# Kernel optimization log

Hardware: AMD Instinct MI355X
Metric: run time of the kernel (lower is better)

The kernel has to match this reference:

```python
import jax, jax.numpy as jnp
import numpy as np

B, T, D = 4, 2048, 512
H, DK = 8, 64  # n_head, d_kv; inner_dim = H*DK = 512


def setup_inputs() -> dict:
    key = jax.random.key(0)
    ks = jax.random.split(key, 6)
    s = 1.0 / np.sqrt(D)
    return {
        "x": jax.random.normal(ks[0], (B, T, D), dtype=jnp.float32),
        "mask": jnp.zeros((B, 1, 1, T), dtype=jnp.float32),
        "position_bias": jax.random.normal(ks[1], (1, H, T, T), dtype=jnp.float32),
        "Wq": jax.random.normal(ks[2], (D, D), dtype=jnp.float32) * s,
        "Wk": jax.random.normal(ks[3], (D, D), dtype=jnp.float32) * s,
        "Wv": jax.random.normal(ks[4], (D, D), dtype=jnp.float32) * s,
        "Wo": jax.random.normal(ks[5], (D, D), dtype=jnp.float32) * s,
    }


def reference(x, mask, position_bias, Wq, Wk, Wv, Wo):
    # Linear projections (torch nn.Linear: y = x @ W.T), split into heads.
    q = (x @ Wq.T).reshape(B, T, H, DK).transpose(0, 2, 1, 3)  # [B,H,T,DK]
    k = (x @ Wk.T).reshape(B, T, H, DK).transpose(0, 2, 1, 3)  # [B,H,S,DK]
    v = (x @ Wv.T).reshape(B, T, H, DK).transpose(0, 2, 1, 3)  # [B,H,S,DK]
    # T5: no 1/sqrt(d_k) scaling; additive position bias + mask before softmax.
    scores = jnp.einsum("bhtd,bhsd->bhts", q, k) + position_bias + mask
    attn = jax.nn.softmax(scores.astype(jnp.float32), axis=-1).astype(q.dtype)
    # dropout is identity at inference
    y = jnp.einsum("bhts,bhsd->bhtd", attn, v)  # [B,H,T,DK]
    y = y.transpose(0, 2, 1, 3).reshape(B, T, H * DK)
    return y @ Wo.T
```

## Files before the change

### kernel.cpp

```cpp
#include <hip/hip_runtime.h>
#include <stdint.h>

typedef unsigned short u16;
typedef __attribute__((ext_vector_type(8))) _Float16 half8;
typedef __attribute__((ext_vector_type(4))) float f32x4;

#define L2E 1.4426950408889634f

#define NTOK 8192
#define DIM  512
#define TT   2048

__device__ __forceinline__ u16 f2h(float f) {
  _Float16 h = (_Float16)f;
  return __builtin_bit_cast(u16, h);
}

__device__ __forceinline__ void async16(const void* g, void* l) {
  __builtin_amdgcn_global_load_lds(
      (const __attribute__((address_space(1))) unsigned int*)g,
      (__attribute__((address_space(3))) unsigned int*)l, 16, 0, 0);
}

__global__ __launch_bounds__(256) void k_convert(
    const float* __restrict__ x, const float* __restrict__ wq,
    const float* __restrict__ wk, const float* __restrict__ wv,
    const float* __restrict__ wo, u16* __restrict__ xb) {
  size_t i = ((size_t)blockIdx.x * 256 + threadIdx.x) * 8;
  const float* src;
  u16* dst;
  size_t off;
  if (i < 4194304) {
    src = x; dst = xb; off = i;
  } else {
    size_t j = i - 4194304;
    int w = (int)(j >> 18);
    off = j & 262143;
    src = (w == 0) ? wq : (w == 1) ? wk : (w == 2) ? wv : wo;
    dst = xb + 4194304 + (size_t)w * 262144;
  }
  float4 a = *(const float4*)(src + off);
  float4 b = *(const float4*)(src + off + 4);
  uint4 pk;
  pk.x = (unsigned)f2h(a.x) | ((unsigned)f2h(a.y) << 16);
  pk.y = (unsigned)f2h(a.z) | ((unsigned)f2h(a.w) << 16);
  pk.z = (unsigned)f2h(b.x) | ((unsigned)f2h(b.y) << 16);
  pk.w = (unsigned)f2h(b.z) | ((unsigned)f2h(b.w) << 16);
  *(uint4*)(dst + off) = pk;
}

template <bool VSWAP>
__global__ __launch_bounds__(256) void k_proj(
    const u16* __restrict__ A, const u16* __restrict__ Wb,
    u16* __restrict__ Db) {
  const int tid = threadIdx.x;
  const int wave = tid >> 6, lane = tid & 63;
  const int quad = lane >> 4, l16 = lane & 15;
  const int wr = wave >> 1, wc = wave & 1;
  const int m0 = blockIdx.x * 128, n0 = blockIdx.y * 128;

  const u16* W;
  u16* D;
  if (VSWAP) {
    W = Wb + 2 * 262144;
    D = Db + 2 * (size_t)4194304;
  } else {
    int z = blockIdx.z;
    W = Wb + (size_t)z * 262144;
    D = Db + (size_t)z * 4194304;
  }

  __shared__ __align__(16) u16 As[128 * 64];
  __shared__ __align__(16) u16 Bs[128 * 64];

  f32x4 acc[4][4];
  for (int rt = 0; rt < 4; ++rt)
    for (int ct = 0; ct < 4; ++ct) acc[rt][ct] = (f32x4){0.f, 0.f, 0.f, 0.f};

  for (int kb = 0; kb < 8; ++kb) {
    const int k0 = kb * 64;
    for (int r = 0; r < 4; ++r) {
      int cid = r * 256 + tid;
      int row = cid >> 3, cl = cid & 7, cg = cl ^ (row & 7);
      async16(A + (size_t)(m0 + row) * DIM + k0 + cg * 8,
              &As[(r * 256 + wave * 64) * 8]);
    }
    for (int r = 0; r < 4; ++r) {
      int cid = r * 256 + tid;
      int row = cid >> 3, cl = cid & 7, cg = cl ^ (row & 7);
      async16(W + (size_t)(n0 + row) * DIM + k0 + cg * 8,
              &Bs[(r * 256 + wave * 64) * 8]);
    }
    __syncthreads();
    for (int kc = 0; kc < 2; ++kc) {
      half8 af[4], wf[4];
      for (int rt = 0; rt < 4; ++rt) {
        int row = wr * 64 + rt * 16 + l16;
        int c = (kc * 4 + quad) ^ (row & 7);
        af[rt] = *(const half8*)&As[row * 64 + c * 8];
      }
      for (int ct = 0; ct < 4; ++ct) {
        int row = wc * 64 + ct * 16 + l16;
        int c = (kc * 4 + quad) ^ (row & 7);
        wf[ct] = *(const half8*)&Bs[row * 64 + c * 8];
      }
      for (int rt = 0; rt < 4; ++rt)
        for (int ct = 0; ct < 4; ++ct)
          acc[rt][ct] = VSWAP
              ? __builtin_amdgcn_mfma_f32_16x16x32_f16(wf[ct], af[rt],
                                                       acc[rt][ct], 0, 0, 0)
              : __builtin_amdgcn_mfma_f32_16x16x32_f16(af[rt], wf[ct],
                                                       acc[rt][ct], 0, 0, 0);
    }
    __syncthreads();
  }

  for (int rt = 0; rt < 4; ++rt)
    for (int ct = 0; ct < 4; ++ct)
      for (int reg = 0; reg < 4; ++reg) {
        float v = acc[rt][ct][reg];
        if (!VSWAP) {
          int gm = m0 + wr * 64 + rt * 16 + quad * 4 + reg;
          int gn = n0 + wc * 64 + ct * 16 + l16;
          int bb = gm >> 11, t = gm & 2047, hh = gn >> 6, dk = gn & 63;
          D[(((size_t)(bb * 8 + hh) * TT + t) << 6) + dk] = f2h(v);
        } else {
          int feat = n0 + wc * 64 + ct * 16 + quad * 4 + reg;
          int tok  = m0 + wr * 64 + rt * 16 + l16;
          int bb = tok >> 11, t = tok & 2047, hh = feat >> 6, dk = feat & 63;
          D[(((size_t)(bb * 8 + hh) << 6) + dk) * TT + t] = f2h(v);
        }
      }
}

__global__ __launch_bounds__(256) void k_ogemm(
    const u16* __restrict__ A, const u16* __restrict__ W,
    float* __restrict__ Df) {
  const int tid = threadIdx.x;
  const int wave = tid >> 6, lane = tid & 63;
  const int quad = lane >> 4, l16 = lane & 15;
  const int wr = wave >> 1, wc = wave & 1;
  const int m0 = blockIdx.x * 64, n0 = blockIdx.y * 128;

  __shared__ __align__(16) u16 As[64 * 64];
  __shared__ __align__(16) u16 Bs[128 * 64];

  f32x4 acc[2][4];
  for (int rt = 0; rt < 2; ++rt)
    for (int ct = 0; ct < 4; ++ct) acc[rt][ct] = (f32x4){0.f, 0.f, 0.f, 0.f};

  for (int kb = 0; kb < 8; ++kb) {
    const int k0 = kb * 64;
    for (int r = 0; r < 2; ++r) {
      int cid = r * 256 + tid;
      int row = cid >> 3, cl = cid & 7, cg = cl ^ (row & 7);
      async16(A + (size_t)(m0 + row) * DIM + k0 + cg * 8,
              &As[(r * 256 + wave * 64) * 8]);
    }
    for (int r = 0; r < 4; ++r) {
      int cid = r * 256 + tid;
      int row = cid >> 3, cl = cid & 7, cg = cl ^ (row & 7);
      async16(W + (size_t)(n0 + row) * DIM + k0 + cg * 8,
              &Bs[(r * 256 + wave * 64) * 8]);
    }
    __syncthreads();
    for (int kc = 0; kc < 2; ++kc) {
      half8 af[2], wf[4];
      for (int rt = 0; rt < 2; ++rt) {
        int row = wr * 32 + rt * 16 + l16;
        int c = (kc * 4 + quad) ^ (row & 7);
        af[rt] = *(const half8*)&As[row * 64 + c * 8];
      }
      for (int ct = 0; ct < 4; ++ct) {
        int row = wc * 64 + ct * 16 + l16;
        int c = (kc * 4 + quad) ^ (row & 7);
        wf[ct] = *(const half8*)&Bs[row * 64 + c * 8];
      }
      for (int rt = 0; rt < 2; ++rt)
        for (int ct = 0; ct < 4; ++ct)
          acc[rt][ct] = __builtin_amdgcn_mfma_f32_16x16x32_f16(
              af[rt], wf[ct], acc[rt][ct], 0, 0, 0);
    }
    __syncthreads();
  }

  for (int rt = 0; rt < 2; ++rt)
    for (int ct = 0; ct < 4; ++ct)
      for (int reg = 0; reg < 4; ++reg) {
        int gm = m0 + wr * 32 + rt * 16 + quad * 4 + reg;
        int gn = n0 + wc * 64 + ct * 16 + l16;
        Df[(size_t)gm * DIM + gn] = acc[rt][ct][reg];
      }
}

__global__ __launch_bounds__(256) void k_attn(
    const u16* __restrict__ Q, const u16* __restrict__ K,
    const u16* __restrict__ Vt, const float* __restrict__ bias,
    const float* __restrict__ mask, u16* __restrict__ Y) {
  const int tid = threadIdx.x;
  const int wv = tid >> 6;
  const int lane = tid & 63;
  const int quad = lane >> 4;
  const int l16 = lane & 15;

  const int bx = blockIdx.x;
  const int bh = bx >> 5;
  const int qt = bx & 31;
  const int b = bh >> 3, h = bh & 7;
  const int q0 = qt * 64;

  __shared__ __align__(16) u16 Ks[64 * 64];
  __shared__ __align__(16) u16 Vs[64 * 64];
  __shared__ __align__(16) u16 Pl[64 * 72];

  half8 qf[2];
  {
    size_t qrow = (size_t)bh * TT + q0 + wv * 16 + l16;
    for (int kc = 0; kc < 2; ++kc)
      qf[kc] = *(const half8*)(Q + qrow * 64 + kc * 32 + quad * 8);
  }

  float m_i[4], l_i[4];
  f32x4 oacc[4];
  for (int r = 0; r < 4; ++r) { m_i[r] = -1e30f; l_i[r] = 0.f; }
  for (int ct = 0; ct < 4; ++ct) oacc[ct] = (f32x4){0.f, 0.f, 0.f, 0.f};

  const size_t biasbase = (size_t)h * TT * TT;

  for (int st = 0; st < 32; ++st) {
    const int s0 = st * 64;
    for (int r = 0; r < 2; ++r) {
      int cid = r * 256 + tid;
      int row = cid >> 3, cl = cid & 7, cg = cl ^ (row & 7);
      async16(K + ((size_t)bh * TT + s0 + row) * 64 + cg * 8,
              &Ks[(r * 256 + wv * 64) * 8]);
      async16(Vt + ((size_t)(bh * 64 + row)) * TT + s0 + cg * 8,
              &Vs[(r * 256 + wv * 64) * 8]);
    }
    __syncthreads();

    float mk[4];
    for (int ct = 0; ct < 4; ++ct) mk[ct] = mask[b * TT + s0 + ct * 16 + l16];

    f32x4 sacc[4];
    for (int ct = 0; ct < 4; ++ct) sacc[ct] = (f32x4){0.f, 0.f, 0.f, 0.f};
    for (int kc = 0; kc < 2; ++kc) {
      half8 kf[4];
      for (int ct = 0; ct < 4; ++ct) {
        int row = ct * 16 + l16;
        int c = (kc * 4 + quad) ^ (row & 7);
        kf[ct] = *(const half8*)&Ks[row * 64 + c * 8];
      }
      for (int ct = 0; ct < 4; ++ct)
        sacc[ct] = __builtin_amdgcn_mfma_f32_16x16x32_f16(
            qf[kc], kf[ct], sacc[ct], 0, 0, 0);
    }

    float bv[4][4];
    {
      int tg = q0 + wv * 16 + quad * 4;
      for (int reg = 0; reg < 4; ++reg) {
        const float* bp = bias + biasbase + (size_t)(tg + reg) * TT + s0 + l16;
        for (int ct = 0; ct < 4; ++ct) bv[ct][reg] = bp[ct * 16];
      }
    }

    for (int reg = 0; reg < 4; ++reg) {
      float s[4];
      for (int ct = 0; ct < 4; ++ct)
        s[ct] = sacc[ct][reg] + bv[ct][reg] + mk[ct];
      float mx = fmaxf(fmaxf(s[0], s[1]), fmaxf(s[2], s[3]));
      mx = fmaxf(mx, __shfl_xor(mx, 1));
      mx = fmaxf(mx, __shfl_xor(mx, 2));
      mx = fmaxf(mx, __shfl_xor(mx, 4));
      mx = fmaxf(mx, __shfl_xor(mx, 8));
      float mold = m_i[reg];
      float mnew = fmaxf(mold, mx);
      float alpha = __builtin_amdgcn_exp2f((mold - mnew) * L2E);
      float p[4], rs = 0.f;
      for (int ct = 0; ct < 4; ++ct) {
        p[ct] = __builtin_amdgcn_exp2f((s[ct] - mnew) * L2E);
        rs += p[ct];
      }
      rs += __shfl_xor(rs, 1);
      rs += __shfl_xor(rs, 2);
      rs += __shfl_xor(rs, 4);
      rs += __shfl_xor(rs, 8);
      l_i[reg] = l_i[reg] * alpha + rs;
      m_i[reg] = mnew;
      for (int ct = 0; ct < 4; ++ct) oacc[ct][reg] *= alpha;
      int prow = wv * 16 + quad * 4 + reg;
      for (int ct = 0; ct < 4; ++ct) Pl[prow * 72 + ct * 16 + l16] = f2h(p[ct]);
    }
    __syncthreads();

    for (int kc = 0; kc < 2; ++kc) {
      half8 pf, vf[4];
      pf = *(const half8*)&Pl[(wv * 16 + l16) * 72 + kc * 32 + quad * 8];
      for (int ct = 0; ct < 4; ++ct) {
        int row = ct * 16 + l16;
        int c = (kc * 4 + quad) ^ (row & 7);
        vf[ct] = *(const half8*)&Vs[row * 64 + c * 8];
      }
      for (int ct = 0; ct < 4; ++ct)
        oacc[ct] = __builtin_amdgcn_mfma_f32_16x16x32_f16(
            pf, vf[ct], oacc[ct], 0, 0, 0);
    }
    __syncthreads();
  }

  for (int reg = 0; reg < 4; ++reg) {
    int tg = q0 + wv * 16 + quad * 4 + reg;
    float inv = 1.f / l_i[reg];
    for (int ct = 0; ct < 4; ++ct) {
      float v = oacc[ct][reg] * inv;
      Y[((size_t)(b * TT + tg)) * DIM + h * 64 + ct * 16 + l16] = f2h(v);
    }
  }
}

extern "C" void kernel_launch(void* const* d_in, const int* in_sizes, int n_in,
                              void* d_out, int out_size, void* d_ws, size_t ws_size,
                              hipStream_t stream) {
  const float* x    = (const float*)d_in[0];
  const float* mask = (const float*)d_in[1];
  const float* bias = (const float*)d_in[2];
  const float* Wq   = (const float*)d_in[3];
  const float* Wk   = (const float*)d_in[4];
  const float* Wv   = (const float*)d_in[5];
  const float* Wo   = (const float*)d_in[6];
  (void)Wk; (void)Wv;

  u16* xb  = (u16*)d_ws;
  u16* wb  = xb + 4194304;
  u16* qkv = wb + 4 * 262144;
  u16* yb  = qkv + 3 * (size_t)4194304;

  k_convert<<<2560, 256, 0, stream>>>(x, Wq, Wk, Wv, Wo, xb);
  k_proj<false><<<dim3(64, 4, 2), 256, 0, stream>>>(xb, wb, qkv);
  k_proj<true><<<dim3(64, 4), 256, 0, stream>>>(xb, wb, qkv);
  k_attn<<<1024, 256, 0, stream>>>(qkv, qkv + 4194304,
                                   qkv + 2 * (size_t)4194304, bias, mask, yb);
  k_ogemm<<<dim3(128, 4), 256, 0, stream>>>(yb, wb + 3 * 262144, (float*)d_out);
}
```

Before: 329.7 us.

## Transpose attention MFMA operands so each lane owns a query row

Swaps the MFMA operand order in the attention kernel so each lane holds one query row across four key columns. Softmax statistics become per-lane scalars reduced with only two cross-lane shuffles, and bias and mask are read as float4 vectors. The next tile's bias is prefetched into registers during the current tile's softmax. The change also replaces a block-wide barrier with a per-wave LDS wait, adds setprio around the MFMA sections and an occupancy hint in launch bounds, and packs P and output stores into 64-bit writes. It risks higher register pressure from the prefetched bias and relies on each wave reading only its own rows of P.

```diff
diff --git a/kernel.cpp b/kernel.cpp
--- a/kernel.cpp
+++ b/kernel.cpp
@@ -193,7 +193,7 @@
       }
 }
 
-__global__ __launch_bounds__(256) void k_attn(
+__global__ __launch_bounds__(256, 4) void k_attn(
     const u16* __restrict__ Q, const u16* __restrict__ K,
     const u16* __restrict__ Vt, const float* __restrict__ bias,
     const float* __restrict__ mask, u16* __restrict__ Y) {
@@ -213,19 +213,23 @@
   __shared__ __align__(16) u16 Vs[64 * 64];
   __shared__ __align__(16) u16 Pl[64 * 72];
 
+  const int qrow = q0 + wv * 16 + l16;
   half8 qf[2];
   {
-    size_t qrow = (size_t)bh * TT + q0 + wv * 16 + l16;
-    for (int kc = 0; kc < 2; ++kc)
-      qf[kc] = *(const half8*)(Q + qrow * 64 + kc * 32 + quad * 8);
-  }
-
-  float m_i[4], l_i[4];
+    size_t qoff = ((size_t)bh * TT + qrow) * 64;
+    qf[0] = *(const half8*)(Q + qoff + quad * 8);
+    qf[1] = *(const half8*)(Q + qoff + 32 + quad * 8);
+  }
+
+  const float* brow = bias + (size_t)h * TT * TT + (size_t)qrow * TT + quad * 4;
+  const float* mrow = mask + (size_t)b * TT + quad * 4;
+
+  float m_i = -1e30f, l_i = 0.f;
   f32x4 oacc[4];
-  for (int r = 0; r < 4; ++r) { m_i[r] = -1e30f; l_i[r] = 0.f; }
   for (int ct = 0; ct < 4; ++ct) oacc[ct] = (f32x4){0.f, 0.f, 0.f, 0.f};
 
-  const size_t biasbase = (size_t)h * TT * TT;
+  f32x4 bL[4];
+  for (int ct = 0; ct < 4; ++ct) bL[ct] = *(const f32x4*)(brow + ct * 16);
 
   for (int st = 0; st < 32; ++st) {
     const int s0 = st * 64;
@@ -237,13 +241,14 @@
       async16(Vt + ((size_t)(bh * 64 + row)) * TT + s0 + cg * 8,
               &Vs[(r * 256 + wv * 64) * 8]);
     }
-    __syncthreads();
-
-    float mk[4];
-    for (int ct = 0; ct < 4; ++ct) mk[ct] = mask[b * TT + s0 + ct * 16 + l16];
+    f32x4 mL[4];
+    for (int ct = 0; ct < 4; ++ct)
+      mL[ct] = *(const f32x4*)(mrow + s0 + ct * 16);
+    __syncthreads();
 
     f32x4 sacc[4];
     for (int ct = 0; ct < 4; ++ct) sacc[ct] = (f32x4){0.f, 0.f, 0.f, 0.f};
+    __builtin_amdgcn_s_setprio(1);
     for (int kc = 0; kc < 2; ++kc) {
       half8 kf[4];
       for (int ct = 0; ct < 4; ++ct) {
@@ -252,70 +257,82 @@
         kf[ct] = *(const half8*)&Ks[row * 64 + c * 8];
       }
       for (int ct = 0; ct < 4; ++ct)
-        sacc[ct] = __builtin_amdgcn_mfma_f32_16x16x32_f16(
-            qf[kc], kf[ct], sacc[ct], 0, 0, 0);
-    }
-
-    float bv[4][4];
+        sacc[ct] = __builtin_amdgcn_mfma_f32_16x16x32_f16(kf[ct], qf[kc],
+                                                          sacc[ct], 0, 0, 0);
+    }
+    __builtin_amdgcn_s_setprio(0);
+
+    float sv[4][4];
+    for (int ct = 0; ct < 4; ++ct)
+      for (int reg = 0; reg < 4; ++reg)
+        sv[ct][reg] = sacc[ct][reg] + bL[ct][reg] + mL[ct][reg];
+
     {
-      int tg = q0 + wv * 16 + quad * 4;
+      int sn = (st < 31) ? s0 + 64 : 0;
+      for (int ct = 0; ct < 4; ++ct)
+        bL[ct] = *(const f32x4*)(brow + sn + ct * 16);
+    }
+
+    float mc[4];
+    for (int ct = 0; ct < 4; ++ct)
+      mc[ct] = fmaxf(fmaxf(sv[ct][0], sv[ct][1]), fmaxf(sv[ct][2], sv[ct][3]));
+    float mx = fmaxf(fmaxf(mc[0], mc[1]), fmaxf(mc[2], mc[3]));
+    mx = fmaxf(mx, __shfl_xor(mx, 16));
+    mx = fmaxf(mx, __shfl_xor(mx, 32));
+    float mnew = fmaxf(m_i, mx);
+    float alpha = __builtin_amdgcn_exp2f((m_i - mnew) * L2E);
+    float nl2e = mnew * L2E;
+    float rs = 0.f;
+    for (int ct = 0; ct < 4; ++ct)
       for (int reg = 0; reg < 4; ++reg) {
-        const float* bp = bias + biasbase + (size_t)(tg + reg) * TT + s0 + l16;
-        for (int ct = 0; ct < 4; ++ct) bv[ct][reg] = bp[ct * 16];
-      }
-    }
-
-    for (int reg = 0; reg < 4; ++reg) {
-      float s[4];
-      for (int ct = 0; ct < 4; ++ct)
-        s[ct] = sacc[ct][reg] + bv[ct][reg] + mk[ct];
-      float mx = fmaxf(fmaxf(s[0], s[1]), fmaxf(s[2], s[3]));
-      mx = fmaxf(mx, __shfl_xor(mx, 1));
-      mx = fmaxf(mx, __shfl_xor(mx, 2));
-      mx = fmaxf(mx, __shfl_xor(mx, 4));
-      mx = fmaxf(mx, __shfl_xor(mx, 8));
-      float mold = m_i[reg];
-      float mnew = fmaxf(mold, mx);
-      float alpha = __builtin_amdgcn_exp2f((mold - mnew) * L2E);
-      float p[4], rs = 0.f;
-      for (int ct = 0; ct < 4; ++ct) {
-        p[ct] = __builtin_amdgcn_exp2f((s[ct] - mnew) * L2E);
-        rs += p[ct];
-      }
-      rs += __shfl_xor(rs, 1);
-      rs += __shfl_xor(rs, 2);
-      rs += __shfl_xor(rs, 4);
-      rs += __shfl_xor(rs, 8);
-      l_i[reg] = l_i[reg] * alpha + rs;
-      m_i[reg] = mnew;
-      for (int ct = 0; ct < 4; ++ct) oacc[ct][reg] *= alpha;
-      int prow = wv * 16 + quad * 4 + reg;
-      for (int ct = 0; ct < 4; ++ct) Pl[prow * 72 + ct * 16 + l16] = f2h(p[ct]);
-    }
-    __syncthreads();
-
+        float p = __builtin_amdgcn_exp2f(sv[ct][reg] * L2E - nl2e);
+        sv[ct][reg] = p;
+        rs += p;
+      }
+    rs += __shfl_xor(rs, 16);
+    rs += __shfl_xor(rs, 32);
+    l_i = l_i * alpha + rs;
+    m_i = mnew;
+    for (int ct = 0; ct < 4; ++ct) {
+      oacc[ct][0] *= alpha; oacc[ct][1] *= alpha;
+      oacc[ct][2] *= alpha; oacc[ct][3] *= alpha;
+    }
+
+    for (int ct = 0; ct < 4; ++ct) {
+      uint2 pk;
+      pk.x = (unsigned)f2h(sv[ct][0]) | ((unsigned)f2h(sv[ct][1]) << 16);
+      pk.y = (unsigned)f2h(sv[ct][2]) | ((unsigned)f2h(sv[ct][3]) << 16);
+      *(uint2*)&Pl[(wv * 16 + l16) * 72 + ct * 16 + quad * 4] = pk;
+    }
+    asm volatile("s_waitcnt lgkmcnt(0)" ::: "memory");
+    __builtin_amdgcn_sched_barrier(0);
+
+    __builtin_amdgcn_s_setprio(1);
     for (int kc = 0; kc < 2; ++kc) {
-      half8 pf, vf[4];
-      pf = *(const half8*)&Pl[(wv * 16 + l16) * 72 + kc * 32 + quad * 8];
+      half8 pf = *(const half8*)&Pl[(wv * 16 + l16) * 72 + kc * 32 + quad * 8];
+      half8 vf[4];
       for (int ct = 0; ct < 4; ++ct) {
         int row = ct * 16 + l16;
         int c = (kc * 4 + quad) ^ (row & 7);
         vf[ct] = *(const half8*)&Vs[row * 64 + c * 8];
       }
       for (int ct = 0; ct < 4; ++ct)
-        oacc[ct] = __builtin_amdgcn_mfma_f32_16x16x32_f16(
-            pf, vf[ct], oacc[ct], 0, 0, 0);
-    }
-    __syncthreads();
-  }
-
-  for (int reg = 0; reg < 4; ++reg) {
-    int tg = q0 + wv * 16 + quad * 4 + reg;
-    float inv = 1.f / l_i[reg];
-    for (int ct = 0; ct < 4; ++ct) {
-      float v = oacc[ct][reg] * inv;
-      Y[((size_t)(b * TT + tg)) * DIM + h * 64 + ct * 16 + l16] = f2h(v);
-    }
+        oacc[ct] = __builtin_amdgcn_mfma_f32_16x16x32_f16(vf[ct], pf,
+                                                          oacc[ct], 0, 0, 0);
+    }
+    __builtin_amdgcn_s_setprio(0);
+    __syncthreads();
+  }
+
+  float inv = 1.f / l_i;
+  size_t ybase = ((size_t)(b * TT + qrow)) * DIM + h * 64 + quad * 4;
+  for (int ct = 0; ct < 4; ++ct) {
+    uint2 pk;
+    pk.x = (unsigned)f2h(oacc[ct][0] * inv) |
+           ((unsigned)f2h(oacc[ct][1] * inv) << 16);
+    pk.y = (unsigned)f2h(oacc[ct][2] * inv) |
+           ((unsigned)f2h(oacc[ct][3] * inv) << 16);
+    *(uint2*)(Y + ybase + ct * 16) = pk;
   }
 }
 
```

New measurement: 322.1 us. -2.3%, faster.
